# Performance work log

Hardware: AMD Instinct MI355X
Metric: run time of the kernel (lower is better)

## Reference

```python
import math
import jax, jax.numpy as jnp
import numpy as np

SQ = 5  # locality window width (static, from init_kwargs)

def _locality_mask_np(hidden_size: int, width: int) -> np.ndarray:
    """[H, H] 0/1 mask: units live on a side x side grid; unit i connects to
    unit j iff their circular (wrap-around) Chebyshev grid distance <= width//2.
    mask_type='circular' -> toroidal wrap."""
    side = int(round(math.sqrt(hidden_size)))
    assert side * side == hidden_size
    r = np.arange(hidden_size) // side
    c = np.arange(hidden_size) % side
    dr = np.abs(r[:, None] - r[None, :])
    dc = np.abs(c[:, None] - c[None, :])
    dr = np.minimum(dr, side - dr)  # circular wrap
    dc = np.minimum(dc, side - dc)
    half = width // 2
    return ((dr <= half) & (dc <= half)).astype(np.float32)


def setup_inputs() -> dict:
    key = jax.random.key(0)
    ks = jax.random.split(key, 8)
    B, S, H = 8, 2048, 1024
    scale = 0.02
    x = jax.random.normal(ks[0], (B, S, H), dtype=jnp.float32)
    Wq = jax.random.normal(ks[1], (H, H), dtype=jnp.float32) * scale
    Wk = jax.random.normal(ks[2], (H, H), dtype=jnp.float32) * scale
    Wv = jax.random.normal(ks[3], (H, H), dtype=jnp.float32) * scale
    bq = jnp.zeros((H,), dtype=jnp.float32)
    bk = jnp.zeros((H,), dtype=jnp.float32)
    bv = jnp.zeros((H,), dtype=jnp.float32)
    Wl = jax.random.normal(ks[4], (H, H), dtype=jnp.float32) * scale
    return {"x": x, "Wq": Wq, "bq": bq, "Wk": Wk, "bk": bk,
            "Wv": Wv, "bv": bv, "Wl": Wl}


def reference(x, Wq, bq, Wk, bk, Wv, bv, Wl):
    H = x.shape[-1]
    mask = jnp.asarray(_locality_mask_np(H, SQ))  # [H, H], static
    # Locally-connected q/k/v projections: dense weight elementwise-masked.
    q = x @ (Wq * mask).T + bq  # [B, S, H]
    k = x @ (Wk * mask).T + bk
    v = x @ (Wv * mask).T + bv
    # Learned spatial querying: locality-masked learned map applied to query.
    q = q @ (Wl * mask).T  # [B, S, H]
    # Manual attention (dropout is identity in eval / p=0).
    scores = jnp.einsum("bsh,bth->bst", q, k) / math.sqrt(H)  # [B, S, S]
    probs = jax.nn.softmax(scores, axis=-1)
    out = jnp.einsum("bst,bth->bsh", probs, v)  # [B, S, H]
    return out, probs
```

## Files before the change

### kernel.cpp

```cpp
#include <hip/hip_runtime.h>

typedef __attribute__((ext_vector_type(8))) short short8;
typedef __attribute__((ext_vector_type(4))) float floatx4;

__device__ __forceinline__ unsigned short f2bf(float f) {
  union { float f; unsigned int u; } x; x.f = f;
  unsigned int r = (x.u + 0x7fffu + ((x.u >> 16) & 1u)) >> 16;
  return (unsigned short)r;
}
__device__ __forceinline__ float bf2f(unsigned short u) {
  union { unsigned int u; float f; } x; x.u = ((unsigned int)u) << 16;
  return x.f;
}

__device__ __forceinline__ void gload_lds16(const void* g, void* l) {
  __builtin_amdgcn_global_load_lds((const __attribute__((address_space(1))) void*)g,
                                   (__attribute__((address_space(3))) void*)l,
                                   16, 0, 0);
}

__global__ __launch_bounds__(128) void prep_weights(
    const float* __restrict__ Wq, const float* __restrict__ Wk,
    const float* __restrict__ Wv, const float* __restrict__ Wl,
    const float* __restrict__ bq, const float* __restrict__ bk,
    const float* __restrict__ bv,
    unsigned short* __restrict__ Wqkv, float* __restrict__ biasAll) {
  const int i = blockIdx.x;
  const int r = i >> 5, c = i & 31;
  const int t = threadIdx.x;
  for (int p = t; p < 1024; p += 128) {
    Wqkv[i * 1024 + p] = 0;
    Wqkv[(1024 + i) * 1024 + p] = 0;
    Wqkv[(2048 + i) * 1024 + p] = 0;
  }
  __syncthreads();
  if (t < 25) {
    int dr = t / 5 - 2, dc = t % 5 - 2;
    int j = (((r + dr) & 31) << 5) | ((c + dc) & 31);
    Wqkv[(1024 + i) * 1024 + j] = f2bf(Wk[i * 1024 + j]);
    Wqkv[(2048 + i) * 1024 + j] = f2bf(Wv[i * 1024 + j]);
  }
  if (t < 81) {
    int dr = t / 9 - 4, dc = t % 9 - 4;
    int j = (((r + dr) & 31) << 5) | ((c + dc) & 31);
    float s = 0.f;
    int erlo = dr - 2 < -2 ? -2 : dr - 2, erhi = dr + 2 > 2 ? 2 : dr + 2;
    int eclo = dc - 2 < -2 ? -2 : dc - 2, echi = dc + 2 > 2 ? 2 : dc + 2;
    for (int er = erlo; er <= erhi; ++er)
      for (int ec = eclo; ec <= echi; ++ec) {
        int m = (((r + er) & 31) << 5) | ((c + ec) & 31);
        s += Wl[i * 1024 + m] * Wq[m * 1024 + j];
      }
    Wqkv[i * 1024 + j] = f2bf(s);
  }
  if (t == 96) {
    float s = 0.f;
    for (int e = 0; e < 25; ++e) {
      int dr = e / 5 - 2, dc = e % 5 - 2;
      int m = (((r + dr) & 31) << 5) | ((c + dc) & 31);
      s += Wl[i * 1024 + m] * bq[m];
    }
    biasAll[i] = s;
  }
  if (t == 97) biasAll[1024 + i] = bk[i];
  if (t == 98) biasAll[2048 + i] = bv[i];
}

__global__ __launch_bounds__(256) void cast_bf16(const float4* __restrict__ x,
                                                 ushort4* __restrict__ xb) {
  int i = blockIdx.x * 256 + threadIdx.x;
  float4 v = x[i];
  ushort4 o;
  o.x = f2bf(v.x); o.y = f2bf(v.y); o.z = f2bf(v.z); o.w = f2bf(v.w);
  xb[i] = o;
}

template <int OUTMODE>
__global__ __launch_bounds__(256, 2) void gemm_bt(
    const unsigned short* __restrict__ A, const unsigned short* __restrict__ B,
    void* __restrict__ Cv, const float* __restrict__ auxc, float* __restrict__ auxw,
    int lda, int ldb, int ldc, int K, float scale,
    size_t sA, size_t sB, size_t sC) {
  __shared__ unsigned short lA[128 * 64];
  __shared__ unsigned short lB[128 * 64];
  __shared__ float sred[2][128];
  const int t = threadIdx.x;
  const int lane = t & 63;
  const int wv = t >> 6;
  const int wm = wv >> 1, wn = wv & 1;
  const int l15 = lane & 15, lq = lane >> 4;
  const int bm = blockIdx.y, bn = blockIdx.x, bz = blockIdx.z;
  A += sA * bz; B += sB * bz;

  floatx4 acc[4][4];
#pragma unroll
  for (int i = 0; i < 4; ++i)
#pragma unroll
    for (int j = 0; j < 4; ++j) acc[i][j] = (floatx4){0.f, 0.f, 0.f, 0.f};

  for (int kt = 0; kt < K; kt += 64) {
    __syncthreads();
#pragma unroll
    for (int c = 0; c < 4; ++c) {
      int slot = c * 256 + t;
      int r = slot >> 3, gp = slot & 7;
      int gd = gp ^ (r & 7);
      gload_lds16(A + (size_t)(bm * 128 + r) * lda + kt + gd * 8,
                  &lA[(size_t)(c * 256 + (t & 192)) * 8]);
      gload_lds16(B + (size_t)(bn * 128 + r) * ldb + kt + gd * 8,
                  &lB[(size_t)(c * 256 + (t & 192)) * 8]);
    }
    __syncthreads();
#pragma unroll
    for (int s = 0; s < 2; ++s) {
      short8 aF[4], bF[4];
#pragma unroll
      for (int i = 0; i < 4; ++i) {
        int rowA = wm * 64 + i * 16 + l15;
        int g = s * 4 + lq;
        aF[i] = *(const short8*)&lA[rowA * 64 + ((g ^ (rowA & 7)) << 3)];
        int rowB = wn * 64 + i * 16 + l15;
        bF[i] = *(const short8*)&lB[rowB * 64 + ((g ^ (rowB & 7)) << 3)];
      }
#pragma unroll
      for (int i = 0; i < 4; ++i)
#pragma unroll
        for (int j = 0; j < 4; ++j)
          acc[i][j] = __builtin_amdgcn_mfma_f32_16x16x32_bf16(aF[i], bF[j],
                                                              acc[i][j], 0, 0, 0);
    }
  }

  const int row0 = bm * 128 + wm * 64;
  const int col0 = bn * 128 + wn * 64;
  if (OUTMODE == 0) {
    unsigned short* C = (unsigned short*)Cv + sC * bz;
#pragma unroll
    for (int i = 0; i < 4; ++i)
#pragma unroll
      for (int j = 0; j < 4; ++j) {
        int col = col0 + j * 16 + l15;
        float bb = auxc[col];
#pragma unroll
        for (int r2 = 0; r2 < 4; ++r2) {
          int row = row0 + i * 16 + (lq << 2) + r2;
          C[(size_t)row * ldc + col] = f2bf(acc[i][j][r2] + bb);
        }
      }
  } else if (OUTMODE == 2) {
    unsigned short* C = (unsigned short*)Cv + sC * bz;
    float p[4][4];
#pragma unroll
    for (int i = 0; i < 4; ++i)
#pragma unroll
      for (int r2 = 0; r2 < 4; ++r2) p[i][r2] = 0.f;
#pragma unroll
    for (int i = 0; i < 4; ++i)
#pragma unroll
      for (int j = 0; j < 4; ++j) {
        int col = col0 + j * 16 + l15;
#pragma unroll
        for (int r2 = 0; r2 < 4; ++r2) {
          int row = row0 + i * 16 + (lq << 2) + r2;
          float e = __expf(acc[i][j][r2] * scale);
          C[(size_t)row * ldc + col] = f2bf(e);
          p[i][r2] += e;
        }
      }
#pragma unroll
    for (int i = 0; i < 4; ++i)
#pragma unroll
      for (int r2 = 0; r2 < 4; ++r2) {
        float v = p[i][r2];
        v += __shfl_xor(v, 1); v += __shfl_xor(v, 2);
        v += __shfl_xor(v, 4); v += __shfl_xor(v, 8);
        p[i][r2] = v;
      }
    __syncthreads();
    if (l15 == 0) {
#pragma unroll
      for (int i = 0; i < 4; ++i)
#pragma unroll
        for (int r2 = 0; r2 < 4; ++r2)
          sred[wn][wm * 64 + i * 16 + (lq << 2) + r2] = p[i][r2];
    }
    __syncthreads();
    if (t < 128) {
      float L = sred[0][t] + sred[1][t];
      auxw[((size_t)bz * 2048 + bm * 128 + t) * 16 + bn] = L;
    }
  } else {
    float* C = (float*)Cv + sC * bz;
#pragma unroll
    for (int i = 0; i < 4; ++i) {
      float il[4];
#pragma unroll
      for (int r2 = 0; r2 < 4; ++r2)
        il[r2] = auxc[(size_t)bz * 2048 + row0 + i * 16 + (lq << 2) + r2];
#pragma unroll
      for (int j = 0; j < 4; ++j) {
        int col = col0 + j * 16 + l15;
#pragma unroll
        for (int r2 = 0; r2 < 4; ++r2) {
          int row = row0 + i * 16 + (lq << 2) + r2;
          C[(size_t)row * ldc + col] = acc[i][j][r2] * il[r2];
        }
      }
    }
  }
}

__global__ __launch_bounds__(1024) void transpose_v(const unsigned short* __restrict__ qkv,
                                                    unsigned short* __restrict__ vT) {
  __shared__ unsigned short tile[32][33];
  int s0 = blockIdx.x * 32, h0 = blockIdx.y * 32, b = blockIdx.z;
  int tx = threadIdx.x, ty = threadIdx.y;
  tile[ty][tx] = qkv[((size_t)b * 2048 + s0 + ty) * 3072 + 2048 + h0 + tx];
  __syncthreads();
  vT[((size_t)b * 1024 + h0 + ty) * 2048 + s0 + tx] = tile[tx][ty];
}

__global__ __launch_bounds__(256) void finish_softmax(
    const float* __restrict__ Lpart, const unsigned short* __restrict__ pb,
    float* __restrict__ invL, float* __restrict__ probs) {
  const size_t row = blockIdx.x;
  const int t = threadIdx.x;
  __shared__ float sInv;
  if (t < 64) {
    float s = (t < 16) ? Lpart[row * 16 + t] : 0.f;
    s += __shfl_xor(s, 1); s += __shfl_xor(s, 2);
    s += __shfl_xor(s, 4); s += __shfl_xor(s, 8);
    if (t == 0) {
      float inv = 1.0f / s;
      sInv = inv;
      invL[row] = inv;
    }
  }
  __syncthreads();
  float inv = sInv;
  const ushort4* pv = (const ushort4*)(pb + row * 2048);
  float4* pr = (float4*)(probs + row * 2048);
  ushort4 a = pv[t * 2], b = pv[t * 2 + 1];
  float4 o0, o1;
  o0.x = bf2f(a.x) * inv; o0.y = bf2f(a.y) * inv;
  o0.z = bf2f(a.z) * inv; o0.w = bf2f(a.w) * inv;
  o1.x = bf2f(b.x) * inv; o1.y = bf2f(b.y) * inv;
  o1.z = bf2f(b.z) * inv; o1.w = bf2f(b.w) * inv;
  pr[t * 2] = o0; pr[t * 2 + 1] = o1;
}

extern "C" void kernel_launch(void* const* d_in, const int* in_sizes, int n_in,
                              void* d_out, int out_size, void* d_ws, size_t ws_size,
                              hipStream_t stream) {
  const float* x  = (const float*)d_in[0];
  const float* Wq = (const float*)d_in[1];
  const float* bq = (const float*)d_in[2];
  const float* Wk = (const float*)d_in[3];
  const float* bk = (const float*)d_in[4];
  const float* Wv = (const float*)d_in[5];
  const float* bv = (const float*)d_in[6];
  const float* Wl = (const float*)d_in[7];

  const int B = 8, S = 2048, H = 1024;
  float* out   = (float*)d_out;
  float* probs = (float*)d_out + (size_t)B * S * H;

  char* ws = (char*)d_ws;
  unsigned short* qkv  = (unsigned short*)(ws + 0);
  unsigned short* pb   = (unsigned short*)(ws + 100663296);
  unsigned short* xb   = (unsigned short*)(ws + 167772160);
  unsigned short* vT   = (unsigned short*)(ws + 167772160);
  unsigned short* Wqkv = (unsigned short*)(ws + 201326592);
  float* biasAll       = (float*)(ws + 207618048);
  float* Lpart         = (float*)(ws + 207630336);
  float* invL          = (float*)(ws + 208678912);

  prep_weights<<<1024, 128, 0, stream>>>(Wq, Wk, Wv, Wl, bq, bk, bv, Wqkv, biasAll);
  cast_bf16<<<16384, 256, 0, stream>>>((const float4*)x, (ushort4*)xb);

  gemm_bt<0><<<dim3(24, 128, 1), 256, 0, stream>>>(xb, Wqkv, qkv, biasAll, nullptr,
      H, H, 3 * H, H, 1.f, 0, 0, 0);

  transpose_v<<<dim3(64, 32, 8), dim3(32, 32), 0, stream>>>(qkv, vT);

  gemm_bt<2><<<dim3(16, 16, 8), 256, 0, stream>>>(qkv, qkv + 1024, pb, nullptr, Lpart,
      3 * H, 3 * H, S, H, 1.0f / 32.0f, (size_t)S * 3 * H, (size_t)S * 3 * H, (size_t)S * S);

  finish_softmax<<<16384, 256, 0, stream>>>(Lpart, pb, invL, probs);

  gemm_bt<3><<<dim3(8, 16, 8), 256, 0, stream>>>(pb, vT, out, invL, nullptr,
      S, S, H, S, 1.0f, (size_t)S * S, (size_t)H * S, (size_t)S * H);
}
```

Measured before the change: 572.4 us.

## Replace 128x128 GEMM with 256x256 double-buffered, 8-wave pipelined MFMA kernel

Replaces the single-buffered 128x128 GEMM with a 256x256 tile, 512-thread kernel. Global-to-LDS loads go into a double buffer and are interleaved across four MFMA sub-phases, using explicit vmcnt/lgkmcnt waits, barriers and s_setprio. The goal is to hide load latency and raise arithmetic intensity per LDS byte. Softmax partial sums fall from 16 to 8 column blocks, and finish_softmax changes to match. The risks are higher register pressure from 32 accumulators per wave, a 128KB LDS footprint, and fewer blocks per launch, which lowers occupancy and CU fill.

```diff
diff --git a/kernel.cpp b/kernel.cpp
--- a/kernel.cpp
+++ b/kernel.cpp
@@ -76,135 +76,220 @@
 }
 
 template <int OUTMODE>
-__global__ __launch_bounds__(256, 2) void gemm_bt(
+__global__ __launch_bounds__(512, 2) void gemm256(
     const unsigned short* __restrict__ A, const unsigned short* __restrict__ B,
     void* __restrict__ Cv, const float* __restrict__ auxc, float* __restrict__ auxw,
     int lda, int ldb, int ldc, int K, float scale,
     size_t sA, size_t sB, size_t sC) {
-  __shared__ unsigned short lA[128 * 64];
-  __shared__ unsigned short lB[128 * 64];
-  __shared__ float sred[2][128];
+  __shared__ __align__(16) unsigned short lds[65536];
   const int t = threadIdx.x;
   const int lane = t & 63;
   const int wv = t >> 6;
-  const int wm = wv >> 1, wn = wv & 1;
+  const int wm = wv >> 2;
+  const int wn = wv & 3;
   const int l15 = lane & 15, lq = lane >> 4;
   const int bm = blockIdx.y, bn = blockIdx.x, bz = blockIdx.z;
   A += sA * bz; B += sB * bz;
 
-  floatx4 acc[4][4];
-#pragma unroll
-  for (int i = 0; i < 4; ++i)
+  const int rl = t >> 3;
+  const int gd = (t & 7) ^ (rl & 7);
+  const int wb = (t >> 6) << 9;
+
+#define STAGE_A(q, tt_)                                                        \
+  gload_lds16(A + (size_t)(bm * 256 + (q) * 64 + rl) * lda + (tt_) * 64 + gd * 8, \
+              &lds[(((tt_) & 1) << 14) + ((q) << 12) + wb])
+#define STAGE_B(q, tt_)                                                        \
+  gload_lds16(B + (size_t)(bn * 256 + (q) * 64 + rl) * ldb + (tt_) * 64 + gd * 8, \
+              &lds[32768 + (((tt_) & 1) << 14) + ((q) << 12) + wb])
+
+  floatx4 acc[8][4];
+#pragma unroll
+  for (int i = 0; i < 8; ++i)
 #pragma unroll
     for (int j = 0; j < 4; ++j) acc[i][j] = (floatx4){0.f, 0.f, 0.f, 0.f};
 
-  for (int kt = 0; kt < K; kt += 64) {
-    __syncthreads();
-#pragma unroll
-    for (int c = 0; c < 4; ++c) {
-      int slot = c * 256 + t;
-      int r = slot >> 3, gp = slot & 7;
-      int gd = gp ^ (r & 7);
-      gload_lds16(A + (size_t)(bm * 128 + r) * lda + kt + gd * 8,
-                  &lA[(size_t)(c * 256 + (t & 192)) * 8]);
-      gload_lds16(B + (size_t)(bn * 128 + r) * ldb + kt + gd * 8,
-                  &lB[(size_t)(c * 256 + (t & 192)) * 8]);
-    }
-    __syncthreads();
-#pragma unroll
-    for (int s = 0; s < 2; ++s) {
-      short8 aF[4], bF[4];
-#pragma unroll
-      for (int i = 0; i < 4; ++i) {
-        int rowA = wm * 64 + i * 16 + l15;
-        int g = s * 4 + lq;
-        aF[i] = *(const short8*)&lA[rowA * 64 + ((g ^ (rowA & 7)) << 3)];
-        int rowB = wn * 64 + i * 16 + l15;
-        bF[i] = *(const short8*)&lB[rowB * 64 + ((g ^ (rowB & 7)) << 3)];
-      }
-#pragma unroll
-      for (int i = 0; i < 4; ++i)
-#pragma unroll
-        for (int j = 0; j < 4; ++j)
-          acc[i][j] = __builtin_amdgcn_mfma_f32_16x16x32_bf16(aF[i], bF[j],
-                                                              acc[i][j], 0, 0, 0);
-    }
-  }
-
-  const int row0 = bm * 128 + wm * 64;
-  const int col0 = bn * 128 + wn * 64;
+  const int NT = K >> 6;
+
+  STAGE_A(0, 0); STAGE_A(1, 0); STAGE_A(2, 0); STAGE_A(3, 0);
+  STAGE_B(0, 0); STAGE_B(1, 0); STAGE_B(2, 0); STAGE_B(3, 0);
+  asm volatile("" ::: "memory");
+  STAGE_A(0, 1); STAGE_A(2, 1);
+  asm volatile("s_waitcnt vmcnt(2)" ::: "memory");
+  __builtin_amdgcn_s_barrier();
+
+  for (int tt = 0; tt < NT; ++tt) {
+    const int bo = (tt & 1) << 14;
+    short8 aF[4][2], bFa[2][2], bFb[2][2];
+
+#pragma unroll
+    for (int i = 0; i < 4; ++i) {
+      int rA = wm * 128 + i * 16 + l15;
+#pragma unroll
+      for (int ks = 0; ks < 2; ++ks) {
+        int g = ks * 4 + lq;
+        aF[i][ks] = *(const short8*)&lds[bo + rA * 64 + ((g ^ (rA & 7)) << 3)];
+      }
+    }
+#pragma unroll
+    for (int j = 0; j < 2; ++j) {
+      int rB = wn * 64 + j * 16 + l15;
+#pragma unroll
+      for (int ks = 0; ks < 2; ++ks) {
+        int g = ks * 4 + lq;
+        bFa[j][ks] = *(const short8*)&lds[32768 + bo + rB * 64 + ((g ^ (rB & 7)) << 3)];
+      }
+    }
+    if (tt + 1 < NT) { STAGE_A(1, tt + 1); STAGE_A(3, tt + 1); STAGE_B(2, tt + 1); STAGE_B(3, tt + 1); }
+    __builtin_amdgcn_s_barrier();
+    __builtin_amdgcn_s_setprio(1);
+#pragma unroll
+    for (int i = 0; i < 4; ++i)
+#pragma unroll
+      for (int j = 0; j < 2; ++j) {
+        acc[i][j] = __builtin_amdgcn_mfma_f32_16x16x32_bf16(aF[i][0], bFa[j][0], acc[i][j], 0, 0, 0);
+        acc[i][j] = __builtin_amdgcn_mfma_f32_16x16x32_bf16(aF[i][1], bFa[j][1], acc[i][j], 0, 0, 0);
+      }
+    __builtin_amdgcn_s_setprio(0);
+    asm volatile("s_waitcnt lgkmcnt(0)" ::: "memory");
+    __builtin_amdgcn_s_barrier();
+
+#pragma unroll
+    for (int j = 0; j < 2; ++j) {
+      int rB = wn * 64 + 32 + j * 16 + l15;
+#pragma unroll
+      for (int ks = 0; ks < 2; ++ks) {
+        int g = ks * 4 + lq;
+        bFb[j][ks] = *(const short8*)&lds[32768 + bo + rB * 64 + ((g ^ (rB & 7)) << 3)];
+      }
+    }
+    if (tt + 1 < NT) { STAGE_B(0, tt + 1); STAGE_B(1, tt + 1); }
+    __builtin_amdgcn_s_barrier();
+    __builtin_amdgcn_s_setprio(1);
+#pragma unroll
+    for (int i = 0; i < 4; ++i)
+#pragma unroll
+      for (int j = 0; j < 2; ++j) {
+        acc[i][2 + j] = __builtin_amdgcn_mfma_f32_16x16x32_bf16(aF[i][0], bFb[j][0], acc[i][2 + j], 0, 0, 0);
+        acc[i][2 + j] = __builtin_amdgcn_mfma_f32_16x16x32_bf16(aF[i][1], bFb[j][1], acc[i][2 + j], 0, 0, 0);
+      }
+    __builtin_amdgcn_s_setprio(0);
+    asm volatile("s_waitcnt lgkmcnt(0)" ::: "memory");
+    __builtin_amdgcn_s_barrier();
+
+#pragma unroll
+    for (int i = 0; i < 4; ++i) {
+      int rA = wm * 128 + 64 + i * 16 + l15;
+#pragma unroll
+      for (int ks = 0; ks < 2; ++ks) {
+        int g = ks * 4 + lq;
+        aF[i][ks] = *(const short8*)&lds[bo + rA * 64 + ((g ^ (rA & 7)) << 3)];
+      }
+    }
+    if (tt + 2 < NT) { STAGE_A(0, tt + 2); STAGE_A(2, tt + 2); }
+    __builtin_amdgcn_s_barrier();
+    __builtin_amdgcn_s_setprio(1);
+#pragma unroll
+    for (int i = 0; i < 4; ++i)
+#pragma unroll
+      for (int j = 0; j < 2; ++j) {
+        acc[4 + i][2 + j] = __builtin_amdgcn_mfma_f32_16x16x32_bf16(aF[i][0], bFb[j][0], acc[4 + i][2 + j], 0, 0, 0);
+        acc[4 + i][2 + j] = __builtin_amdgcn_mfma_f32_16x16x32_bf16(aF[i][1], bFb[j][1], acc[4 + i][2 + j], 0, 0, 0);
+      }
+    __builtin_amdgcn_s_setprio(0);
+    asm volatile("s_waitcnt lgkmcnt(0)" ::: "memory");
+    __builtin_amdgcn_s_barrier();
+
+    __builtin_amdgcn_s_setprio(1);
+#pragma unroll
+    for (int i = 0; i < 4; ++i)
+#pragma unroll
+      for (int j = 0; j < 2; ++j) {
+        acc[4 + i][j] = __builtin_amdgcn_mfma_f32_16x16x32_bf16(aF[i][0], bFa[j][0], acc[4 + i][j], 0, 0, 0);
+        acc[4 + i][j] = __builtin_amdgcn_mfma_f32_16x16x32_bf16(aF[i][1], bFa[j][1], acc[4 + i][j], 0, 0, 0);
+      }
+    __builtin_amdgcn_s_setprio(0);
+    if (tt < NT - 2)       { asm volatile("s_waitcnt vmcnt(2)" ::: "memory"); }
+    else if (tt == NT - 2) { asm volatile("s_waitcnt vmcnt(0)" ::: "memory"); }
+    __builtin_amdgcn_s_barrier();
+  }
+#undef STAGE_A
+#undef STAGE_B
+
+  const int row0 = bm * 256 + wm * 128;
+  const int col0 = bn * 256 + wn * 64;
+
   if (OUTMODE == 0) {
     unsigned short* C = (unsigned short*)Cv + sC * bz;
 #pragma unroll
-    for (int i = 0; i < 4; ++i)
-#pragma unroll
-      for (int j = 0; j < 4; ++j) {
-        int col = col0 + j * 16 + l15;
+    for (int m = 0; m < 8; ++m) {
+      int rb = row0 + ((m >> 2) << 6) + ((m & 3) << 4) + (lq << 2);
+#pragma unroll
+      for (int n = 0; n < 4; ++n) {
+        int col = col0 + ((n >> 1) << 5) + ((n & 1) << 4) + l15;
         float bb = auxc[col];
 #pragma unroll
-        for (int r2 = 0; r2 < 4; ++r2) {
-          int row = row0 + i * 16 + (lq << 2) + r2;
-          C[(size_t)row * ldc + col] = f2bf(acc[i][j][r2] + bb);
-        }
-      }
+        for (int r2 = 0; r2 < 4; ++r2)
+          C[(size_t)(rb + r2) * ldc + col] = f2bf(acc[m][n][r2] + bb);
+      }
+    }
   } else if (OUTMODE == 2) {
     unsigned short* C = (unsigned short*)Cv + sC * bz;
-    float p[4][4];
-#pragma unroll
-    for (int i = 0; i < 4; ++i)
-#pragma unroll
-      for (int r2 = 0; r2 < 4; ++r2) p[i][r2] = 0.f;
-#pragma unroll
-    for (int i = 0; i < 4; ++i)
-#pragma unroll
-      for (int j = 0; j < 4; ++j) {
-        int col = col0 + j * 16 + l15;
+    float p[8][4];
+#pragma unroll
+    for (int m = 0; m < 8; ++m)
+#pragma unroll
+      for (int r2 = 0; r2 < 4; ++r2) p[m][r2] = 0.f;
+#pragma unroll
+    for (int m = 0; m < 8; ++m) {
+      int rb = row0 + ((m >> 2) << 6) + ((m & 3) << 4) + (lq << 2);
+#pragma unroll
+      for (int n = 0; n < 4; ++n) {
+        int col = col0 + ((n >> 1) << 5) + ((n & 1) << 4) + l15;
 #pragma unroll
         for (int r2 = 0; r2 < 4; ++r2) {
-          int row = row0 + i * 16 + (lq << 2) + r2;
-          float e = __expf(acc[i][j][r2] * scale);
-          C[(size_t)row * ldc + col] = f2bf(e);
-          p[i][r2] += e;
+          float e = __expf(acc[m][n][r2] * scale);
+          C[(size_t)(rb + r2) * ldc + col] = f2bf(e);
+          p[m][r2] += e;
         }
       }
-#pragma unroll
-    for (int i = 0; i < 4; ++i)
+    }
+#pragma unroll
+    for (int m = 0; m < 8; ++m)
 #pragma unroll
       for (int r2 = 0; r2 < 4; ++r2) {
-        float v = p[i][r2];
+        float v = p[m][r2];
         v += __shfl_xor(v, 1); v += __shfl_xor(v, 2);
         v += __shfl_xor(v, 4); v += __shfl_xor(v, 8);
-        p[i][r2] = v;
-      }
+        p[m][r2] = v;
+      }
+    float* sred = (float*)lds;
+    if (l15 == 0) {
+#pragma unroll
+      for (int m = 0; m < 8; ++m)
+#pragma unroll
+        for (int r2 = 0; r2 < 4; ++r2)
+          sred[wn * 256 + wm * 128 + ((m >> 2) << 6) + ((m & 3) << 4) + (lq << 2) + r2] = p[m][r2];
+    }
     __syncthreads();
-    if (l15 == 0) {
-#pragma unroll
-      for (int i = 0; i < 4; ++i)
-#pragma unroll
-        for (int r2 = 0; r2 < 4; ++r2)
-          sred[wn][wm * 64 + i * 16 + (lq << 2) + r2] = p[i][r2];
-    }
-    __syncthreads();
-    if (t < 128) {
-      float L = sred[0][t] + sred[1][t];
-      auxw[((size_t)bz * 2048 + bm * 128 + t) * 16 + bn] = L;
+    if (t < 256) {
+      float L = sred[t] + sred[256 + t] + sred[512 + t] + sred[768 + t];
+      auxw[((size_t)bz * 2048 + bm * 256 + t) * 8 + bn] = L;
     }
   } else {
     float* C = (float*)Cv + sC * bz;
 #pragma unroll
-    for (int i = 0; i < 4; ++i) {
+    for (int m = 0; m < 8; ++m) {
+      int rb = row0 + ((m >> 2) << 6) + ((m & 3) << 4) + (lq << 2);
       float il[4];
 #pragma unroll
       for (int r2 = 0; r2 < 4; ++r2)
-        il[r2] = auxc[(size_t)bz * 2048 + row0 + i * 16 + (lq << 2) + r2];
-#pragma unroll
-      for (int j = 0; j < 4; ++j) {
-        int col = col0 + j * 16 + l15;
-#pragma unroll
-        for (int r2 = 0; r2 < 4; ++r2) {
-          int row = row0 + i * 16 + (lq << 2) + r2;
-          C[(size_t)row * ldc + col] = acc[i][j][r2] * il[r2];
-        }
+        il[r2] = auxc[(size_t)bz * 2048 + rb + r2];
+#pragma unroll
+      for (int n = 0; n < 4; ++n) {
+        int col = col0 + ((n >> 1) << 5) + ((n & 1) << 4) + l15;
+#pragma unroll
+        for (int r2 = 0; r2 < 4; ++r2)
+          C[(size_t)(rb + r2) * ldc + col] = acc[m][n][r2] * il[r2];
       }
     }
   }
@@ -227,9 +312,8 @@
   const int t = threadIdx.x;
   __shared__ float sInv;
   if (t < 64) {
-    float s = (t < 16) ? Lpart[row * 16 + t] : 0.f;
-    s += __shfl_xor(s, 1); s += __shfl_xor(s, 2);
-    s += __shfl_xor(s, 4); s += __shfl_xor(s, 8);
+    float s = (t < 8) ? Lpart[row * 8 + t] : 0.f;
+    s += __shfl_xor(s, 1); s += __shfl_xor(s, 2); s += __shfl_xor(s, 4);
     if (t == 0) {
       float inv = 1.0f / s;
       sInv = inv;
@@ -278,16 +362,16 @@
   prep_weights<<<1024, 128, 0, stream>>>(Wq, Wk, Wv, Wl, bq, bk, bv, Wqkv, biasAll);
   cast_bf16<<<16384, 256, 0, stream>>>((const float4*)x, (ushort4*)xb);
 
-  gemm_bt<0><<<dim3(24, 128, 1), 256, 0, stream>>>(xb, Wqkv, qkv, biasAll, nullptr,
+  gemm256<0><<<dim3(12, 64, 1), 512, 0, stream>>>(xb, Wqkv, qkv, biasAll, nullptr,
       H, H, 3 * H, H, 1.f, 0, 0, 0);
 
   transpose_v<<<dim3(64, 32, 8), dim3(32, 32), 0, stream>>>(qkv, vT);
 
-  gemm_bt<2><<<dim3(16, 16, 8), 256, 0, stream>>>(qkv, qkv + 1024, pb, nullptr, Lpart,
+  gemm256<2><<<dim3(8, 8, 8), 512, 0, stream>>>(qkv, qkv + 1024, pb, nullptr, Lpart,
       3 * H, 3 * H, S, H, 1.0f / 32.0f, (size_t)S * 3 * H, (size_t)S * 3 * H, (size_t)S * S);
 
   finish_softmax<<<16384, 256, 0, stream>>>(Lpart, pb, invL, probs);
 
-  gemm_bt<3><<<dim3(8, 16, 8), 256, 0, stream>>>(pb, vT, out, invL, nullptr,
+  gemm256<3><<<dim3(4, 8, 8), 512, 0, stream>>>(pb, vT, out, invL, nullptr,
       S, S, H, S, 1.0f, (size_t)S * S, (size_t)H * S, (size_t)S * H);
 }
```

Result: faster. 550.3 us (-3.9%).
